# Performance work log

Hardware: AMD Instinct MI355X
Metric: run time of the kernel (lower is better)

## Reference

```python
import jax, jax.numpy as jnp
import numpy as np

NU, NI, DIN, DH, L, NNZ = 100000, 50000, 64, 128, 2, 5000000
SLOPE = 0.2  # LeakyReLU negative slope (args['p'])
EPS = 1e-5


def setup_inputs() -> dict:
    key = jax.random.key(0)
    ks = jax.random.split(key, 10)
    return {
        'emb_table': jax.random.normal(ks[0], (NU + NI, DIN), jnp.float32) * 0.1,
        'fc_u_w': jax.random.normal(ks[1], (DH, DIN), jnp.float32) * 0.01,
        'fc_u_b': jnp.zeros((DH,), jnp.float32),
        'fc_i_w': jax.random.normal(ks[2], (DH, DIN), jnp.float32) * 0.01,
        'fc_i_b': jnp.zeros((DH,), jnp.float32),
        'vals': jax.random.uniform(ks[3], (NNZ,), jnp.float32),
        'Wu': jax.random.normal(ks[4], (L, DH, DH), jnp.float32) * 0.01,
        'ln1g_u': jnp.ones((L, DH), jnp.float32),
        'ln1b_u': jnp.zeros((L, DH), jnp.float32),
        'ln2g_u': jnp.ones((L, DH), jnp.float32),
        'ln2b_u': jnp.zeros((L, DH), jnp.float32),
        'Wi': jax.random.normal(ks[5], (L, DH, DH), jnp.float32) * 0.01,
        'ln1g_i': jnp.ones((L, DH), jnp.float32),
        'ln1b_i': jnp.zeros((L, DH), jnp.float32),
        'ln2g_i': jnp.ones((L, DH), jnp.float32),
        'ln2b_i': jnp.zeros((L, DH), jnp.float32),
        'rows': jax.random.randint(ks[6], (NNZ,), 0, NU, jnp.int32),
        'cols': jax.random.randint(ks[7], (NNZ,), 0, NI, jnp.int32),
    }


def layer_norm(x, g, b):
    mu = jnp.mean(x, axis=-1, keepdims=True)
    xc = x - mu
    var = jnp.mean(xc * xc, axis=-1, keepdims=True)
    return xc * jax.lax.rsqrt(var + EPS) * g + b


def spmm(r, c, vals, x, n_out):
    # out[r] += vals * x[c]   (sparse [n_out, n_c] @ dense [n_c, d])
    return jax.ops.segment_sum(vals[:, None] * x[c], r, num_segments=n_out)


def hconv(r, c, vals, n_r, n_c, x, W, g1, b1, g2, b2):
    # HGNNConv: ln1(fc(spmm(A^T, x))) then leaky(ln2(spmm(A, lat1)))
    y1 = spmm(c, r, vals, x, n_c)            # [n_c, DH] = A^T x
    lat1 = layer_norm(y1 @ W.T, g1, b1)       # fc bias=False
    y2 = spmm(r, c, vals, lat1, n_r)          # [n_r, DH] = A lat1
    return jax.nn.leaky_relu(layer_norm(y2, g2, b2), SLOPE)


def reference(emb_table, fc_u_w, fc_u_b, fc_i_w, fc_i_b, vals,
              Wu, ln1g_u, ln1b_u, ln2g_u, ln2b_u,
              Wi, ln1g_i, ln1b_i, ln2g_i, ln2b_i,
              rows, cols):
    leaky = lambda x: jax.nn.leaky_relu(x, SLOPE)
    # dropout is identity in eval mode
    u = leaky(emb_table[:NU] @ fc_u_w.T + fc_u_b)   # [NU, DH]
    i = leaky(emb_table[NU:] @ fc_i_w.T + fc_i_b)   # [NI, DH]
    acc = jnp.concatenate([u, i], axis=0)
    for k in range(L):
        hu = hconv(rows, cols, vals, NU, NI, u,
                   Wu[k], ln1g_u[k], ln1b_u[k], ln2g_u[k], ln2b_u[k])
        hi = hconv(cols, rows, vals, NI, NU, i,
                   Wi[k], ln1g_i[k], ln1b_i[k], ln2g_i[k], ln2b_i[k])
        u = u + hu
        i = i + hi
        acc = acc + jnp.concatenate([hu, hi], axis=0)
    all_emb = acc / jnp.float32(L + 1)  # mean over stacked layer outputs
    return all_emb[:NU], all_emb[NU:]
```

## Files before the change

### kernel.cpp

```cpp
#include <hip/hip_runtime.h>
#include <math.h>

namespace {

constexpr int kNU = 100000;
constexpr int kNI = 50000;
constexpr int kDIN = 64;
constexpr int kDH = 128;
constexpr int kDH2 = kDH / 2;
constexpr int kNNZ = 5000000;
constexpr float kSlope = 0.2f;
constexpr float kEps = 1e-5f;

constexpr int kNSeg = kNU + kNI;
constexpr int kScanTile = 2048;
constexpr int kScanBlocks = (kNSeg + kScanTile - 1) / kScanTile;

struct alignas(8) Edge { int idx; float val; };

__device__ inline float2 bf2f(uint p) {
  return make_float2(__uint_as_float(p << 16),
                     __uint_as_float(p & 0xffff0000u));
}
__device__ inline uint f2bf1(float f) {
  const uint a = __float_as_uint(f);
  return (a + 0x7fffu + ((a >> 16) & 1u)) >> 16;
}
__device__ inline uint f2bf(float2 v) {
  return f2bf1(v.x) | (f2bf1(v.y) << 16);
}

__device__ inline void fma8(float* acc, uint4 s, float v) {
  float2 p;
  p = bf2f(s.x); acc[0] = fmaf(v, p.x, acc[0]); acc[1] = fmaf(v, p.y, acc[1]);
  p = bf2f(s.y); acc[2] = fmaf(v, p.x, acc[2]); acc[3] = fmaf(v, p.y, acc[3]);
  p = bf2f(s.z); acc[4] = fmaf(v, p.x, acc[4]); acc[5] = fmaf(v, p.y, acc[5]);
  p = bf2f(s.w); acc[6] = fmaf(v, p.x, acc[6]); acc[7] = fmaf(v, p.y, acc[7]);
}

__device__ inline uint4 pack8(const float* acc) {
  uint4 o;
  o.x = f2bf(make_float2(acc[0], acc[1]));
  o.y = f2bf(make_float2(acc[2], acc[3]));
  o.z = f2bf(make_float2(acc[4], acc[5]));
  o.w = f2bf(make_float2(acc[6], acc[7]));
  return o;
}

__global__ __launch_bounds__(128) void fc_in_kernel(
    const float* __restrict__ emb, const float* __restrict__ wu,
    const float* __restrict__ bu, const float* __restrict__ wi,
    const float* __restrict__ bi, uint* __restrict__ ubuf,
    uint* __restrict__ ibuf, float* __restrict__ out) {
  const int n = blockIdx.x;
  const int d = threadIdx.x;
  __shared__ float e[kDIN];
  __shared__ float sh[kDH];
  if (d < kDIN) e[d] = emb[(size_t)n * kDIN + d];
  __syncthreads();
  const float* W;
  const float* B;
  uint* dst;
  int nl;
  if (n < kNU) { W = wu; B = bu; dst = ubuf; nl = n; }
  else         { W = wi; B = bi; dst = ibuf; nl = n - kNU; }
  float s = B[d];
  const float* wr = W + (size_t)d * kDIN;
#pragma unroll
  for (int k = 0; k < kDIN; ++k) s = fmaf(e[k], wr[k], s);
  s = s > 0.f ? s : kSlope * s;
  sh[d] = s;
  out[(size_t)n * kDH + d] = s;
  __syncthreads();
  if (d < kDH2)
    dst[(size_t)nl * kDH2 + d] = f2bf(make_float2(sh[2 * d], sh[2 * d + 1]));
}

__global__ __launch_bounds__(256) void hist_kernel(
    const int* __restrict__ rows, const int* __restrict__ cols,
    int* __restrict__ cnt) {
  const int e = blockIdx.x * 256 + threadIdx.x;
  if (e >= kNNZ) return;
  atomicAdd(&cnt[rows[e]], 1);
  atomicAdd(&cnt[kNU + cols[e]], 1);
}

__global__ __launch_bounds__(256) void scan_partial_kernel(
    const int* __restrict__ in, int* __restrict__ out, int* __restrict__ bsum,
    int N) {
  __shared__ int sdata[256];
  const int tid = threadIdx.x;
  const int base = blockIdx.x * kScanTile + tid * 8;
  int v[8];
  int s = 0;
#pragma unroll
  for (int j = 0; j < 8; ++j) {
    v[j] = (base + j < N) ? in[base + j] : 0;
    s += v[j];
  }
  sdata[tid] = s;
  __syncthreads();
#pragma unroll
  for (int off = 1; off < 256; off <<= 1) {
    int t = (tid >= off) ? sdata[tid - off] : 0;
    __syncthreads();
    sdata[tid] += t;
    __syncthreads();
  }
  int run = sdata[tid] - s;
#pragma unroll
  for (int j = 0; j < 8; ++j) {
    if (base + j < N) out[base + j] = run;
    run += v[j];
  }
  if (tid == 255) bsum[blockIdx.x] = sdata[255];
}

__global__ __launch_bounds__(256) void scan_bsums_kernel(int* __restrict__ bsum,
                                                         int M) {
  __shared__ int sd[256];
  const int tid = threadIdx.x;
  const int v = (tid < M) ? bsum[tid] : 0;
  sd[tid] = v;
  __syncthreads();
#pragma unroll
  for (int off = 1; off < 256; off <<= 1) {
    int t = (tid >= off) ? sd[tid - off] : 0;
    __syncthreads();
    sd[tid] += t;
    __syncthreads();
  }
  if (tid < M) bsum[tid] = sd[tid] - v;
}

__global__ __launch_bounds__(256) void scan_add_kernel(
    int* __restrict__ out, const int* __restrict__ bsum, int N) {
  const int i = blockIdx.x * 256 + threadIdx.x;
  if (i < N) out[i] += bsum[i / kScanTile];
  if (i == 0) out[N] = 2 * kNNZ;
}

__global__ __launch_bounds__(256) void scatter_kernel(
    const int* __restrict__ rows, const int* __restrict__ cols,
    const float* __restrict__ vals, int* __restrict__ cur,
    Edge* __restrict__ edges) {
  const int e = blockIdx.x * 256 + threadIdx.x;
  if (e >= kNNZ) return;
  const int r = rows[e];
  const int c = cols[e];
  const float v = vals[e];
  const int p = atomicAdd(&cur[r], 1);
  *(int2*)&edges[p] = make_int2(c, __float_as_int(v));
  const int q = atomicAdd(&cur[kNU + c], 1);
  *(int2*)&edges[q] = make_int2(r, __float_as_int(v));
}

__global__ __launch_bounds__(256) void spmm_g1_kernel(
    uint* __restrict__ dst, const uint* __restrict__ src,
    const int* __restrict__ ptr, const Edge* __restrict__ edges, int N) {
  const int sub = threadIdx.x >> 4;
  const int l16 = threadIdx.x & 15;
  const int n = blockIdx.x * 16 + sub;
  if (n >= N) return;
  const int off = l16 << 2;
  int e = ptr[n];
  const int e1 = ptr[n + 1];
  float acc[8] = {0.f, 0.f, 0.f, 0.f, 0.f, 0.f, 0.f, 0.f};
  for (; e + 2 <= e1; e += 2) {
    const Edge r0 = edges[e];
    const Edge r1 = edges[e + 1];
    const uint4 s0 = *(const uint4*)(src + (size_t)r0.idx * kDH2 + off);
    const uint4 s1 = *(const uint4*)(src + (size_t)r1.idx * kDH2 + off);
    fma8(acc, s0, r0.val);
    fma8(acc, s1, r1.val);
  }
  if (e < e1) {
    const Edge r = edges[e];
    const uint4 s = *(const uint4*)(src + (size_t)r.idx * kDH2 + off);
    fma8(acc, s, r.val);
  }
  *(uint4*)(dst + (size_t)n * kDH2 + off) = pack8(acc);
}

__global__ __launch_bounds__(256) void spmm_g2_kernel(
    uint* __restrict__ dstA, const uint* __restrict__ srcA,
    uint* __restrict__ dstB, const uint* __restrict__ srcB,
    const int* __restrict__ ptr, const Edge* __restrict__ edges, int N) {
  const int sub = threadIdx.x >> 4;
  const int l16 = threadIdx.x & 15;
  const int n = blockIdx.x * 16 + sub;
  if (n >= N) return;
  const int off = l16 << 2;
  int e = ptr[n];
  const int e1 = ptr[n + 1];
  float aA[8] = {0.f, 0.f, 0.f, 0.f, 0.f, 0.f, 0.f, 0.f};
  float aB[8] = {0.f, 0.f, 0.f, 0.f, 0.f, 0.f, 0.f, 0.f};
  for (; e + 2 <= e1; e += 2) {
    const Edge r0 = edges[e];
    const Edge r1 = edges[e + 1];
    const uint4 a0 = *(const uint4*)(srcA + (size_t)r0.idx * kDH2 + off);
    const uint4 b0 = *(const uint4*)(srcB + (size_t)r0.idx * kDH2 + off);
    const uint4 a1 = *(const uint4*)(srcA + (size_t)r1.idx * kDH2 + off);
    const uint4 b1 = *(const uint4*)(srcB + (size_t)r1.idx * kDH2 + off);
    fma8(aA, a0, r0.val);
    fma8(aB, b0, r0.val);
    fma8(aA, a1, r1.val);
    fma8(aB, b1, r1.val);
  }
  if (e < e1) {
    const Edge r = edges[e];
    const uint4 a = *(const uint4*)(srcA + (size_t)r.idx * kDH2 + off);
    const uint4 b = *(const uint4*)(srcB + (size_t)r.idx * kDH2 + off);
    fma8(aA, a, r.val);
    fma8(aB, b, r.val);
  }
  *(uint4*)(dstA + (size_t)n * kDH2 + off) = pack8(aA);
  *(uint4*)(dstB + (size_t)n * kDH2 + off) = pack8(aB);
}

constexpr int kFclnRows = 8;
constexpr int kWPad = 132;

__global__ __launch_bounds__(256) void fcln_kernel(
    const uint* __restrict__ X, const float* __restrict__ W,
    const float* __restrict__ g, const float* __restrict__ b,
    uint* __restrict__ out, int N) {
  __shared__ float Wt[kDH * kWPad];
  __shared__ float Xl[kFclnRows][kDH];
  const int tid = threadIdx.x;
  for (int idx = tid; idx < kDH * kDH; idx += 256) {
    const int d = idx >> 7, k = idx & 127;
    Wt[k * kWPad + d] = W[idx];
  }
  const int row0 = blockIdx.x * kFclnRows;
  const int r = tid >> 5;
  const int l = tid & 31;
  {
    const int n = row0 + r;
    uint2 xv = make_uint2(0u, 0u);
    if (n < N) xv = *(const uint2*)(X + (size_t)n * kDH2 + l * 2);
    const float2 p0 = bf2f(xv.x);
    const float2 p1 = bf2f(xv.y);
    Xl[r][l * 4 + 0] = p0.x;
    Xl[r][l * 4 + 1] = p0.y;
    Xl[r][l * 4 + 2] = p1.x;
    Xl[r][l * 4 + 3] = p1.y;
  }
  __syncthreads();
  float4 acc = make_float4(0.f, 0.f, 0.f, 0.f);
  const int d0 = l * 4;
#pragma unroll 4
  for (int k = 0; k < kDH; ++k) {
    const float x = Xl[r][k];
    const float4 w = *(const float4*)(&Wt[k * kWPad + d0]);
    acc.x = fmaf(x, w.x, acc.x);
    acc.y = fmaf(x, w.y, acc.y);
    acc.z = fmaf(x, w.z, acc.z);
    acc.w = fmaf(x, w.w, acc.w);
  }
  float s = acc.x + acc.y + acc.z + acc.w;
  float sq = acc.x * acc.x + acc.y * acc.y + acc.z * acc.z + acc.w * acc.w;
#pragma unroll
  for (int m = 16; m >= 1; m >>= 1) {
    s += __shfl_xor(s, m, 32);
    sq += __shfl_xor(sq, m, 32);
  }
  const float mu = s * (1.f / kDH);
  const float var = sq * (1.f / kDH) - mu * mu;
  const float rs = 1.f / sqrtf(var + kEps);
  const int n = row0 + r;
  if (n < N) {
    const float4 gg = *(const float4*)(g + d0);
    const float4 bb = *(const float4*)(b + d0);
    float2 o0, o1;
    o0.x = (acc.x - mu) * rs * gg.x + bb.x;
    o0.y = (acc.y - mu) * rs * gg.y + bb.y;
    o1.x = (acc.z - mu) * rs * gg.z + bb.z;
    o1.y = (acc.w - mu) * rs * gg.w + bb.w;
    *(uint2*)(out + (size_t)n * kDH2 + l * 2) = make_uint2(f2bf(o0), f2bf(o1));
  }
}

__global__ __launch_bounds__(256) void leaky_ln_kernel(
    const uint* __restrict__ T, const float* __restrict__ g,
    const float* __restrict__ b, uint* __restrict__ upd,
    float* __restrict__ acc, int N) {
  const int wid = threadIdx.x >> 6;
  const int lane = threadIdx.x & 63;
  const int n = blockIdx.x * 4 + wid;
  if (n >= N) return;
  const float2 v = bf2f(T[(size_t)n * kDH2 + lane]);
  float s = v.x + v.y;
  float sq = v.x * v.x + v.y * v.y;
#pragma unroll
  for (int m = 32; m >= 1; m >>= 1) {
    s += __shfl_xor(s, m, 64);
    sq += __shfl_xor(sq, m, 64);
  }
  const float mu = s * (1.f / kDH);
  const float var = sq * (1.f / kDH) - mu * mu;
  const float rs = 1.f / sqrtf(var + kEps);
  const int d = lane * 2;
  const float2 gg = *(const float2*)(g + d);
  const float2 bb = *(const float2*)(b + d);
  float hx = (v.x - mu) * rs * gg.x + bb.x;
  float hy = (v.y - mu) * rs * gg.y + bb.y;
  hx = hx > 0.f ? hx : kSlope * hx;
  hy = hy > 0.f ? hy : kSlope * hy;
  float2 uv = bf2f(upd[(size_t)n * kDH2 + lane]);
  uv.x += hx;
  uv.y += hy;
  upd[(size_t)n * kDH2 + lane] = f2bf(uv);
  float2 av = *(const float2*)(acc + (size_t)n * kDH + d);
  av.x += hx;
  av.y += hy;
  *(float2*)(acc + (size_t)n * kDH + d) = av;
}

__global__ __launch_bounds__(256) void scale_kernel(float* __restrict__ p,
                                                    float sc, int n4) {
  const int gid = blockIdx.x * 256 + threadIdx.x;
  if (gid < n4) {
    float4 v = ((float4*)p)[gid];
    v.x *= sc; v.y *= sc; v.z *= sc; v.w *= sc;
    ((float4*)p)[gid] = v;
  }
}

}

extern "C" void kernel_launch(void* const* d_in, const int* in_sizes, int n_in,
                              void* d_out, int out_size, void* d_ws,
                              size_t ws_size, hipStream_t stream) {
  const float* emb    = (const float*)d_in[0];
  const float* fc_u_w = (const float*)d_in[1];
  const float* fc_u_b = (const float*)d_in[2];
  const float* fc_i_w = (const float*)d_in[3];
  const float* fc_i_b = (const float*)d_in[4];
  const float* vals   = (const float*)d_in[5];
  const float* Wu     = (const float*)d_in[6];
  const float* ln1g_u = (const float*)d_in[7];
  const float* ln1b_u = (const float*)d_in[8];
  const float* ln2g_u = (const float*)d_in[9];
  const float* ln2b_u = (const float*)d_in[10];
  const float* Wi     = (const float*)d_in[11];
  const float* ln1g_i = (const float*)d_in[12];
  const float* ln1b_i = (const float*)d_in[13];
  const float* ln2g_i = (const float*)d_in[14];
  const float* ln2b_i = (const float*)d_in[15];
  const int*   rows   = (const int*)d_in[16];
  const int*   cols   = (const int*)d_in[17];
  float* out = (float*)d_out;

  uint* bufU = (uint*)d_ws;
  uint* bufI = bufU + (size_t)kNU * kDH2;
  uint* P    = bufI + (size_t)kNI * kDH2;
  uint* Q    = P + (size_t)kNU * kDH2;
  uint* R    = Q + (size_t)kNU * kDH2;
  Edge* edges = (Edge*)(R + (size_t)kNU * kDH2);
  int*  cnt  = (int*)(edges + (size_t)2 * kNNZ);
  int*  ptr  = cnt + kNSeg;
  int*  cur  = ptr + kNSeg + 1;
  int*  bsum = cur + kNSeg + 1;

  const int egrid = (kNNZ + 255) / 256;
  const int gridU = (kNU + 15) / 16;
  const int gridI = (kNI + 15) / 16;
  const int lgridU = (kNU + 3) / 4;
  const int lgridI = (kNI + 3) / 4;
  const int fgridU = (kNU + kFclnRows - 1) / kFclnRows;
  const int fgridI = (kNI + kFclnRows - 1) / kFclnRows;

  hipMemsetAsync(cnt, 0, (size_t)kNSeg * sizeof(int), stream);
  hist_kernel<<<egrid, 256, 0, stream>>>(rows, cols, cnt);
  scan_partial_kernel<<<kScanBlocks, 256, 0, stream>>>(cnt, ptr, bsum, kNSeg);
  scan_bsums_kernel<<<1, 256, 0, stream>>>(bsum, kScanBlocks);
  scan_add_kernel<<<(kNSeg + 255) / 256, 256, 0, stream>>>(ptr, bsum, kNSeg);
  hipMemcpyAsync(cur, ptr, (size_t)(kNSeg + 1) * sizeof(int),
                 hipMemcpyDeviceToDevice, stream);
  scatter_kernel<<<egrid, 256, 0, stream>>>(rows, cols, vals, cur, edges);

  fc_in_kernel<<<kNU + kNI, 128, 0, stream>>>(emb, fc_u_w, fc_u_b, fc_i_w,
                                              fc_i_b, bufU, bufI, out);

  spmm_g1_kernel<<<gridI, 256, 0, stream>>>(P, bufU, ptr + kNU, edges, kNI);
  fcln_kernel<<<fgridI, 256, 0, stream>>>(P, Wu, ln1g_u, ln1b_u, Q, kNI);
  spmm_g2_kernel<<<gridU, 256, 0, stream>>>(P, Q, R, bufI, ptr, edges, kNU);
  leaky_ln_kernel<<<lgridU, 256, 0, stream>>>(P, ln2g_u, ln2b_u, bufU, out,
                                              kNU);
  fcln_kernel<<<fgridU, 256, 0, stream>>>(R, Wi, ln1g_i, ln1b_i, Q, kNU);
  spmm_g2_kernel<<<gridI, 256, 0, stream>>>(P, Q, R, bufU, ptr + kNU, edges,
                                            kNI);
  leaky_ln_kernel<<<lgridI, 256, 0, stream>>>(P, ln2g_i, ln2b_i, bufI,
                                              out + (size_t)kNU * kDH, kNI);
  fcln_kernel<<<fgridI, 256, 0, stream>>>(R, Wu + kDH * kDH, ln1g_u + kDH,
                                          ln1b_u + kDH, Q, kNI);
  spmm_g2_kernel<<<gridU, 256, 0, stream>>>(P, Q, R, bufI, ptr, edges, kNU);
  leaky_ln_kernel<<<lgridU, 256, 0, stream>>>(P, ln2g_u + kDH, ln2b_u + kDH,
                                              bufU, out, kNU);
  fcln_kernel<<<fgridU, 256, 0, stream>>>(R, Wi + kDH * kDH, ln1g_i + kDH,
                                          ln1b_i + kDH, Q, kNU);
  spmm_g1_kernel<<<gridI, 256, 0, stream>>>(P, Q, ptr + kNU, edges, kNI);
  leaky_ln_kernel<<<lgridI, 256, 0, stream>>>(P, ln2g_i + kDH, ln2b_i + kDH,
                                              bufI, out + (size_t)kNU * kDH,
                                              kNI);

  const int n4 = (kNU + kNI) * kDH / 4;
  scale_kernel<<<(n4 + 255) / 256, 256, 0, stream>>>(out, 1.f / 3.f, n4);
}
```

Measured before the change: 3.457 ms.

## Replace global-atomic CSR scatter with two-pass bucketed binning through shared memory

The direct scatter used one global atomic per edge endpoint and wrote to random locations in the edge array. It is replaced by two passes. The first bins edges into 1024-segment buckets in LDS and flushes each bucket's records contiguously to a staging area reused from the workspace. The second places records per bucket using LDS atomics. This aims to cut global atomic contention and random-write traffic during CSR construction, at the cost of an extra pass over the staging data and more kernel launches.

```diff
diff --git a/kernel.cpp b/kernel.cpp
--- a/kernel.cpp
+++ b/kernel.cpp
@@ -15,6 +15,12 @@
 constexpr int kNSeg = kNU + kNI;
 constexpr int kScanTile = 2048;
 constexpr int kScanBlocks = (kNSeg + kScanTile - 1) / kScanTile;
+
+constexpr int kBktShift = 10;
+constexpr int kBktSegs = 1 << kBktShift;
+constexpr int kNBkt = (kNSeg + kBktSegs - 1) >> kBktShift;
+constexpr int kP1Edges = 2048;
+constexpr int kP1Rec = kP1Edges * 2;
 
 struct alignas(8) Edge { int idx; float val; };
 
@@ -140,19 +146,94 @@
   if (i == 0) out[N] = 2 * kNNZ;
 }
 
-__global__ __launch_bounds__(256) void scatter_kernel(
+__global__ __launch_bounds__(256) void init_gcur_kernel(
+    int* __restrict__ gcur, const int* __restrict__ ptr) {
+  const int b = blockIdx.x * 256 + threadIdx.x;
+  if (b < kNBkt) gcur[b] = ptr[b << kBktShift];
+}
+
+__global__ __launch_bounds__(256) void p1_bin_kernel(
     const int* __restrict__ rows, const int* __restrict__ cols,
-    const float* __restrict__ vals, int* __restrict__ cur,
+    const float* __restrict__ vals, int* __restrict__ gcur,
+    uint2* __restrict__ staging) {
+  __shared__ uint2 rec[kP1Rec];
+  __shared__ int offs[kNBkt + 1];
+  __shared__ int slot[kNBkt];
+  __shared__ int sc[256];
+  const int tid = threadIdx.x;
+  const int e0 = blockIdx.x * kP1Edges;
+  const int ne = min(kP1Edges, kNNZ - e0);
+
+  if (tid <= kNBkt) offs[tid] = 0;
+  __syncthreads();
+  for (int j = tid; j < ne; j += 256) {
+    const int r = rows[e0 + j];
+    const int c = cols[e0 + j];
+    atomicAdd(&offs[r >> kBktShift], 1);
+    atomicAdd(&offs[(kNU + c) >> kBktShift], 1);
+  }
+  __syncthreads();
+  const int v = (tid < kNBkt) ? offs[tid] : 0;
+  sc[tid] = v;
+  __syncthreads();
+#pragma unroll
+  for (int off = 1; off < 256; off <<= 1) {
+    int t = (tid >= off) ? sc[tid - off] : 0;
+    __syncthreads();
+    sc[tid] += t;
+    __syncthreads();
+  }
+  const int run = sc[tid] - v;
+  __syncthreads();
+  if (tid < kNBkt) { offs[tid] = run; slot[tid] = run; }
+  if (tid == 255) offs[kNBkt] = sc[255];
+  __syncthreads();
+  for (int j = tid; j < ne; j += 256) {
+    const int r = rows[e0 + j];
+    const int c = cols[e0 + j];
+    const uint vb = __float_as_uint(vals[e0 + j]);
+    int b = r >> kBktShift;
+    int p = atomicAdd(&slot[b], 1);
+    rec[p] = make_uint2(((uint)c << kBktShift) | (uint)(r & (kBktSegs - 1)), vb);
+    const int s2 = kNU + c;
+    b = s2 >> kBktShift;
+    p = atomicAdd(&slot[b], 1);
+    rec[p] = make_uint2(((uint)r << kBktShift) | (uint)(s2 & (kBktSegs - 1)), vb);
+  }
+  __syncthreads();
+  const int wid = tid >> 6;
+  const int lane = tid & 63;
+  for (int b = wid; b < kNBkt; b += 4) {
+    const int o = offs[b];
+    const int csize = offs[b + 1] - o;
+    if (csize == 0) continue;
+    int gb;
+    if (lane == 0) gb = atomicAdd(&gcur[b], csize);
+    gb = __shfl(gb, 0, 64);
+    for (int r2 = lane; r2 < csize; r2 += 64) staging[gb + r2] = rec[o + r2];
+  }
+}
+
+__global__ __launch_bounds__(512) void p2_place_kernel(
+    const uint2* __restrict__ staging, const int* __restrict__ ptr,
     Edge* __restrict__ edges) {
-  const int e = blockIdx.x * 256 + threadIdx.x;
-  if (e >= kNNZ) return;
-  const int r = rows[e];
-  const int c = cols[e];
-  const float v = vals[e];
-  const int p = atomicAdd(&cur[r], 1);
-  *(int2*)&edges[p] = make_int2(c, __float_as_int(v));
-  const int q = atomicAdd(&cur[kNU + c], 1);
-  *(int2*)&edges[q] = make_int2(r, __float_as_int(v));
+  __shared__ int curr[kBktSegs];
+  const int b = blockIdx.x;
+  const int seg0 = b << kBktShift;
+  const int segend = min(seg0 + kBktSegs, kNSeg);
+  const int nseg = segend - seg0;
+  const int tid = threadIdx.x;
+  for (int s = tid; s < nseg; s += 512) curr[s] = ptr[seg0 + s];
+  __syncthreads();
+  const int rbeg = ptr[seg0];
+  const int rend = ptr[segend];
+  for (int r = rbeg + tid; r < rend; r += 512) {
+    const uint2 rc = staging[r];
+    const int sl = rc.x & (kBktSegs - 1);
+    const int idx = rc.x >> kBktShift;
+    const int p = atomicAdd(&curr[sl], 1);
+    *(int2*)&edges[p] = make_int2(idx, (int)rc.y);
+  }
 }
 
 __global__ __launch_bounds__(256) void spmm_g1_kernel(
@@ -357,11 +438,12 @@
   uint* P    = bufI + (size_t)kNI * kDH2;
   uint* Q    = P + (size_t)kNU * kDH2;
   uint* R    = Q + (size_t)kNU * kDH2;
+  uint2* staging = (uint2*)d_ws;
   Edge* edges = (Edge*)(R + (size_t)kNU * kDH2);
   int*  cnt  = (int*)(edges + (size_t)2 * kNNZ);
   int*  ptr  = cnt + kNSeg;
-  int*  cur  = ptr + kNSeg + 1;
-  int*  bsum = cur + kNSeg + 1;
+  int*  bsum = ptr + kNSeg + 1;
+  int*  gcur = bsum + kScanBlocks;
 
   const int egrid = (kNNZ + 255) / 256;
   const int gridU = (kNU + 15) / 16;
@@ -376,9 +458,10 @@
   scan_partial_kernel<<<kScanBlocks, 256, 0, stream>>>(cnt, ptr, bsum, kNSeg);
   scan_bsums_kernel<<<1, 256, 0, stream>>>(bsum, kScanBlocks);
   scan_add_kernel<<<(kNSeg + 255) / 256, 256, 0, stream>>>(ptr, bsum, kNSeg);
-  hipMemcpyAsync(cur, ptr, (size_t)(kNSeg + 1) * sizeof(int),
-                 hipMemcpyDeviceToDevice, stream);
-  scatter_kernel<<<egrid, 256, 0, stream>>>(rows, cols, vals, cur, edges);
+  init_gcur_kernel<<<(kNBkt + 255) / 256, 256, 0, stream>>>(gcur, ptr);
+  p1_bin_kernel<<<(kNNZ + kP1Edges - 1) / kP1Edges, 256, 0, stream>>>(
+      rows, cols, vals, gcur, staging);
+  p2_place_kernel<<<kNBkt, 512, 0, stream>>>(staging, ptr, edges);
 
   fc_in_kernel<<<kNU + kNI, 128, 0, stream>>>(emb, fc_u_w, fc_u_b, fc_i_w,
                                               fc_i_b, bufU, bufI, out);
```

Result: slower. 4.663 ms (+34.9%).
